# Kernel tuning notes

Measured on AMD Instinct MI355X. Metric: run time of the kernel, lower is better.

The kernel has to match this reference:

```python
import jax, jax.numpy as jnp
import numpy as np

H = 1024          # hidden_size
NH = 16           # num_attention_heads
HD = H // NH      # attention_head_size (= rotary_dim)
I = 4096          # intermediate_size
E = 8             # num_experts
TOPK = 2          # top_k_experts
EPS = 1e-12       # layer_norm_eps
B, S = 2, 2048


def setup_inputs() -> dict:
    key = jax.random.key(0)
    ks = jax.random.split(key, 12)
    sc = 0.02
    return {
        "hidden_states": jax.random.normal(ks[0], (B, S, H), dtype=jnp.float32),
        "Wq": jax.random.normal(ks[1], (H, H), dtype=jnp.float32) * sc,
        "Wk": jax.random.normal(ks[2], (H, H), dtype=jnp.float32) * sc,
        "Wv": jax.random.normal(ks[3], (H, H), dtype=jnp.float32) * sc,
        "Wd": jax.random.normal(ks[4], (H, H), dtype=jnp.float32) * sc,
        "bd": jnp.zeros((H,), dtype=jnp.float32),
        "ln1_g": jnp.ones((H,), dtype=jnp.float32),
        "ln1_b": jnp.zeros((H,), dtype=jnp.float32),
        "Wg": jax.random.normal(ks[5], (H, E), dtype=jnp.float32) * sc,
        "W1": jax.random.normal(ks[6], (E, H, I), dtype=jnp.float32) * sc,
        "W2": jax.random.normal(ks[7], (E, I, H), dtype=jnp.float32) * sc,
        "ln2_g": jnp.ones((H,), dtype=jnp.float32),
        "ln2_b": jnp.zeros((H,), dtype=jnp.float32),
    }


def _layernorm(x, g, b):
    mu = jnp.mean(x, axis=-1, keepdims=True)
    var = jnp.mean(jnp.square(x - mu), axis=-1, keepdims=True)
    return (x - mu) * jax.lax.rsqrt(var + EPS) * g + b


def _rotate_half(x):
    x1, x2 = x[..., : HD // 2], x[..., HD // 2 :]
    return jnp.concatenate((-x2, x1), axis=-1)


def _rope_cos_sin(seq_len, dtype):
    inv_freq = 1.0 / (10000.0 ** (jnp.arange(0, HD, 2, dtype=jnp.float32) / HD))
    t = jnp.arange(seq_len, dtype=jnp.float32)
    freqs = jnp.einsum("i,j->ij", t, inv_freq)          # [S, HD/2]
    emb = jnp.concatenate((freqs, freqs), axis=-1)        # [S, HD]
    return jnp.cos(emb).astype(dtype)[None, None], jnp.sin(emb).astype(dtype)[None, None]


def reference(hidden_states, Wq, Wk, Wv, Wd, bd, ln1_g, ln1_b, Wg, W1, W2, ln2_g, ln2_b):
    b, s, h = hidden_states.shape
    x = hidden_states

    # ---- multi-head attention with RoPE ----
    def heads(z):  # [B,S,H] -> [B,NH,S,HD]
        return z.reshape(b, s, NH, HD).transpose(0, 2, 1, 3)

    q = heads(x @ Wq)
    k = heads(x @ Wk)
    v = heads(x @ Wv)
    cos, sin = _rope_cos_sin(s, q.dtype)
    q = q * cos + _rotate_half(q) * sin
    k = k * cos + _rotate_half(k) * sin

    scores = jnp.einsum("bnqd,bnkd->bnqk", q, k) / jnp.sqrt(jnp.float32(HD)).astype(q.dtype)
    probs = jax.nn.softmax(scores, axis=-1)
    ctx = jnp.einsum("bnqk,bnkd->bnqd", probs, v)
    ctx = ctx.transpose(0, 2, 1, 3).reshape(b, s, h)

    attn_out = ctx @ Wd + bd
    hs = _layernorm(attn_out + x, ln1_g, ln1_b)  # residual + LN

    # ---- MoE ----
    T = b * s
    xt = hs.reshape(T, h)
    router_logits = xt @ Wg                                   # [T, E]
    probs_r = jax.nn.softmax(router_logits.astype(jnp.float32), axis=-1)
    rw, sel = jax.lax.top_k(probs_r, TOPK)                    # [T, K]
    rw = rw / jnp.sum(rw, axis=-1, keepdims=True)

    # aux load-balancing loss
    f_i = jnp.sum(jax.nn.one_hot(sel, E, dtype=jnp.float32), axis=(0, 1)) / T
    P_i = jnp.mean(probs_r, axis=0)
    aux_loss = E * jnp.sum(f_i * P_i)

    # per-token combine weights [T, E] (0 for unrouted experts)
    combine = jnp.zeros((T, E), dtype=jnp.float32)
    combine = combine.at[jnp.arange(T)[:, None], sel].add(rw)
    combine = combine.astype(xt.dtype)

    moe_out = jnp.zeros_like(xt)
    for e in range(E):  # small fixed expert loop
        ye = jax.nn.gelu(xt @ W1[e], approximate=False) @ W2[e]
        moe_out = moe_out + combine[:, e : e + 1] * ye
    moe_out = moe_out.reshape(b, s, h)

    out = _layernorm(hs + moe_out, ln2_g, ln2_b)
    return out, aux_loss
```

## Files before the change

kernel.cpp:

```cpp
#include <hip/hip_runtime.h>
#include <hip/hip_bf16.h>
#include <math.h>

#define H_ 1024
#define NH_ 16
#define HD_ 64
#define I_ 4096
#define E_ 8
#define B_ 2
#define S_ 2048
#define T_ 4096

#define MAXSLOTS 9216
#define MAXTILES 72

typedef __attribute__((ext_vector_type(8))) short short8v;
typedef __attribute__((ext_vector_type(4))) float f32x4;

#define GLOAD16(g, l) __builtin_amdgcn_global_load_lds((const __attribute__((address_space(1))) void*)(g), (__attribute__((address_space(3))) void*)(l), 16, 0, 0)

static __device__ inline unsigned short f2bf(float x) {
    __hip_bfloat16 h = __float2bfloat16(x);
    unsigned short u;
    __builtin_memcpy(&u, &h, 2);
    return u;
}
static __device__ inline float bf2f(unsigned short u) {
    __hip_bfloat16 h;
    __builtin_memcpy(&h, &u, 2);
    return __bfloat162float(h);
}

static __device__ inline float gelu_fast(float x) {
    float z  = x * 0.70710678118654752f;
    float az = fabsf(z);
    float t  = __builtin_amdgcn_rcpf(fmaf(0.3275911f, az, 1.f));
    float p  = fmaf(1.061405429f, t, -1.453152027f);
    p = fmaf(p, t, 1.421413741f);
    p = fmaf(p, t, -0.284496736f);
    p = fmaf(p, t, 0.254829592f);
    p = p * t;
    float e = __expf(-az*az);
    float er = 1.f - p*e;
    er = (z < 0.f) ? -er : er;
    return 0.5f * x * (1.f + er);
}

__global__ void zero_all(float* __restrict__ p, int n, float* __restrict__ misc16) {
    int i = blockIdx.x * blockDim.x + threadIdx.x;
    if (i < n) p[i] = 0.f;
    if (blockIdx.x == 0 && threadIdx.x < 16) misc16[threadIdx.x] = 0.f;
}

__global__ __launch_bounds__(256) void prep_inputs(
    const float* __restrict__ x,
    const float* __restrict__ Wq, const float* __restrict__ Wk,
    const float* __restrict__ Wv, const float* __restrict__ Wd,
    __hip_bfloat16* __restrict__ xa_hi, __hip_bfloat16* __restrict__ xa_lo,
    __hip_bfloat16* __restrict__ wqkv_h, __hip_bfloat16* __restrict__ wqkv_l,
    __hip_bfloat16* __restrict__ wd_h, __hip_bfloat16* __restrict__ wd_l)
{
    __shared__ float t[64][65];
    const int bid = blockIdx.x;
    const int tid = threadIdx.x;
    if (bid < 4096) {
        int i = bid * 256 + tid;
        float4 v = ((const float4*)x)[i];
        unsigned short h0 = f2bf(v.x), h1 = f2bf(v.y), h2 = f2bf(v.z), h3 = f2bf(v.w);
        unsigned short l0 = f2bf(v.x - bf2f(h0)), l1 = f2bf(v.y - bf2f(h1));
        unsigned short l2 = f2bf(v.z - bf2f(h2)), l3 = f2bf(v.w - bf2f(h3));
        uint2 ph = make_uint2((unsigned)h0 | ((unsigned)h1 << 16), (unsigned)h2 | ((unsigned)h3 << 16));
        uint2 pl = make_uint2((unsigned)l0 | ((unsigned)l1 << 16), (unsigned)l2 | ((unsigned)l3 << 16));
        *(uint2*)((char*)xa_hi + (size_t)i*8) = ph;
        *(uint2*)((char*)xa_lo + (size_t)i*8) = pl;
        return;
    }
    int tt = bid - 4096;
    int bx = tt & 15, by = (tt >> 4) & 15, z = tt >> 8;
    const float* in = (z==0) ? Wq : (z==1) ? Wk : (z==2) ? Wv : Wd;
    __hip_bfloat16* oh = (z<3) ? (wqkv_h + (size_t)z*1024*1024) : wd_h;
    __hip_bfloat16* ol = (z<3) ? (wqkv_l + (size_t)z*1024*1024) : wd_l;
    int k0 = by*64, n0 = bx*64;
    #pragma unroll
    for (int it=0; it<4; ++it) {
        int lin = it*256 + tid;
        int r = lin >> 4, c4 = (lin & 15) << 2;
        float4 v = *(const float4*)&in[(size_t)(k0+r)*1024 + n0 + c4];
        t[r][c4] = v.x; t[r][c4+1] = v.y; t[r][c4+2] = v.z; t[r][c4+3] = v.w;
    }
    __syncthreads();
    #pragma unroll
    for (int it=0; it<4; ++it) {
        int lin = it*256 + tid;
        int r = lin >> 4, c4 = (lin & 15) << 2;
        float v0 = t[c4][r], v1 = t[c4+1][r], v2 = t[c4+2][r], v3 = t[c4+3][r];
        ushort4 hh, ll;
        hh.x = f2bf(v0); hh.y = f2bf(v1); hh.z = f2bf(v2); hh.w = f2bf(v3);
        ll.x = f2bf(v0 - bf2f(hh.x)); ll.y = f2bf(v1 - bf2f(hh.y));
        ll.z = f2bf(v2 - bf2f(hh.z)); ll.w = f2bf(v3 - bf2f(hh.w));
        size_t o = (size_t)(n0+r)*1024 + k0 + c4;
        *(ushort4*)&oh[o] = hh;
        *(ushort4*)&ol[o] = ll;
    }
}

__global__ __launch_bounds__(256) void transpose_bf16(
    const float* __restrict__ in, __hip_bfloat16* __restrict__ outp, int K, int N)
{
    __shared__ float t[64][65];
    size_t eoff = (size_t)blockIdx.z * (size_t)K * (size_t)N;
    int k0 = blockIdx.y*64, n0 = blockIdx.x*64;
    int tid = threadIdx.x;
    #pragma unroll
    for (int it=0; it<4; ++it) {
        int lin = it*256 + tid;
        int r = lin >> 4, c4 = (lin & 15) << 2;
        float4 v = *(const float4*)&in[eoff + (size_t)(k0+r)*N + n0 + c4];
        t[r][c4] = v.x; t[r][c4+1] = v.y; t[r][c4+2] = v.z; t[r][c4+3] = v.w;
    }
    __syncthreads();
    #pragma unroll
    for (int it=0; it<4; ++it) {
        int lin = it*256 + tid;
        int r = lin >> 4, c4 = (lin & 15) << 2;
        ushort4 o;
        o.x = f2bf(t[c4][r]);   o.y = f2bf(t[c4+1][r]);
        o.z = f2bf(t[c4+2][r]); o.w = f2bf(t[c4+3][r]);
        *(ushort4*)&outp[eoff + (size_t)(n0+r)*K + k0 + c4] = o;
    }
}

template<bool BIAS>
__global__ __launch_bounds__(256, 2) void gemm_bf16x3(
    const __hip_bfloat16* __restrict__ Ah, const __hip_bfloat16* __restrict__ Al,
    const __hip_bfloat16* __restrict__ Bh, const __hip_bfloat16* __restrict__ Bl,
    float* __restrict__ C, const float* __restrict__ bias, int N, int K, int nbx)
{
    const int tid = threadIdx.x;
    const int w = tid >> 6, lane = tid & 63;
    const int wg = blockIdx.x;
    const int xcd = wg & 7, ix = wg >> 3;
    const int byc = (int)(gridDim.x >> 3) / nbx;
    const int by = xcd*byc + ix / nbx;
    const int bx = ix % nbx;

    __shared__ __align__(16) char smem[65536];
    const int AH = 0, AL = 16384, BH = 32768, BL = 49152;

    const int laneg = lane >> 3;
    const int k2sw = ((lane & 7) ^ laneg) << 4;
    const int l15 = lane & 15, l4 = lane >> 4;
    const int wr = w >> 1, wc = w & 1;

    f32x4 acc[4][4];
    #pragma unroll
    for (int m=0;m<4;m++)
        #pragma unroll
        for (int n=0;n<4;n++) acc[m][n] = (f32x4){0.f,0.f,0.f,0.f};

    for (int k0 = 0; k0 < K; k0 += 64) {
        __syncthreads();
        #pragma unroll
        for (int qq=0;qq<4;qq++) {
            int arow = by*128 + (w*4+qq)*8 + laneg;
            int brow = bx*128 + (w*4+qq)*8 + laneg;
            size_t aoff = ((size_t)arow*K + k0)*2 + k2sw;
            size_t boff = ((size_t)brow*K + k0)*2 + k2sw;
            GLOAD16((const char*)Ah + aoff, smem + AH + (w*4+qq)*1024);
            GLOAD16((const char*)Al + aoff, smem + AL + (w*4+qq)*1024);
            GLOAD16((const char*)Bh + boff, smem + BH + (w*4+qq)*1024);
            GLOAD16((const char*)Bl + boff, smem + BL + (w*4+qq)*1024);
        }
        __syncthreads();

        short8v ahf[4][2], alf[4][2], bhf[4][2], blf[4][2];
        #pragma unroll
        for (int m=0;m<4;m++) {
            int row = wr*64 + m*16 + l15;
            int rb = row << 7, rsw = (row & 7) << 4;
            #pragma unroll
            for (int s=0;s<2;s++) {
                int off = rb + ((s*64 + (l4<<4)) ^ rsw);
                ahf[m][s] = *(const short8v*)(smem + AH + off);
                alf[m][s] = *(const short8v*)(smem + AL + off);
            }
        }
        #pragma unroll
        for (int n=0;n<4;n++) {
            int row = wc*64 + n*16 + l15;
            int rb = row << 7, rsw = (row & 7) << 4;
            #pragma unroll
            for (int s=0;s<2;s++) {
                int off = rb + ((s*64 + (l4<<4)) ^ rsw);
                bhf[n][s] = *(const short8v*)(smem + BH + off);
                blf[n][s] = *(const short8v*)(smem + BL + off);
            }
        }
        #pragma unroll
        for (int m=0;m<4;m++)
            #pragma unroll
            for (int n=0;n<4;n++)
                #pragma unroll
                for (int s=0;s<2;s++) {
                    acc[m][n] = __builtin_amdgcn_mfma_f32_16x16x32_bf16(ahf[m][s], bhf[n][s], acc[m][n], 0, 0, 0);
                    acc[m][n] = __builtin_amdgcn_mfma_f32_16x16x32_bf16(ahf[m][s], blf[n][s], acc[m][n], 0, 0, 0);
                    acc[m][n] = __builtin_amdgcn_mfma_f32_16x16x32_bf16(alf[m][s], bhf[n][s], acc[m][n], 0, 0, 0);
                }
    }

    #pragma unroll
    for (int m=0;m<4;m++)
        #pragma unroll
        for (int j=0;j<4;j++) {
            int orow = by*128 + wr*64 + m*16 + l4*4 + j;
            #pragma unroll
            for (int n=0;n<4;n++) {
                int ocol = bx*128 + wc*64 + n*16 + l15;
                float v = acc[m][n][j];
                if (BIAS) v += bias[ocol];
                C[(size_t)orow*N + ocol] = v;
            }
        }
}

__global__ __launch_bounds__(256, 2) void fused_qkv_w12(
    const __hip_bfloat16* __restrict__ Ah, const __hip_bfloat16* __restrict__ Al,
    const __hip_bfloat16* __restrict__ Bh, const __hip_bfloat16* __restrict__ Bl,
    float* __restrict__ C,
    const float* __restrict__ W1, const float* __restrict__ W2,
    __hip_bfloat16* __restrict__ W1t, __hip_bfloat16* __restrict__ W2t)
{
    __shared__ __align__(16) char smem[65536];
    const int tid = threadIdx.x;
    const int bid = blockIdx.x;

    if (bid < 768) {
        const int N = 3072, K = 1024;
        const int w = tid >> 6, lane = tid & 63;
        const int xcd = bid & 7, ix = bid >> 3;
        const int by = xcd*4 + ix / 24;
        const int bx = ix % 24;
        const int AH = 0, AL = 16384, BH = 32768, BL = 49152;
        const int laneg = lane >> 3;
        const int k2sw = ((lane & 7) ^ laneg) << 4;
        const int l15 = lane & 15, l4 = lane >> 4;
        const int wr = w >> 1, wc = w & 1;

        f32x4 acc[4][4];
        #pragma unroll
        for (int m=0;m<4;m++)
            #pragma unroll
            for (int n=0;n<4;n++) acc[m][n] = (f32x4){0.f,0.f,0.f,0.f};

        for (int k0 = 0; k0 < K; k0 += 64) {
            __syncthreads();
            #pragma unroll
            for (int qq=0;qq<4;qq++) {
                int arow = by*128 + (w*4+qq)*8 + laneg;
                int brow = bx*128 + (w*4+qq)*8 + laneg;
                size_t aoff = ((size_t)arow*K + k0)*2 + k2sw;
                size_t boff = ((size_t)brow*K + k0)*2 + k2sw;
                GLOAD16((const char*)Ah + aoff, smem + AH + (w*4+qq)*1024);
                GLOAD16((const char*)Al + aoff, smem + AL + (w*4+qq)*1024);
                GLOAD16((const char*)Bh + boff, smem + BH + (w*4+qq)*1024);
                GLOAD16((const char*)Bl + boff, smem + BL + (w*4+qq)*1024);
            }
            __syncthreads();

            short8v ahf[4][2], alf[4][2], bhf[4][2], blf[4][2];
            #pragma unroll
            for (int m=0;m<4;m++) {
                int row = wr*64 + m*16 + l15;
                int rb = row << 7, rsw = (row & 7) << 4;
                #pragma unroll
                for (int s=0;s<2;s++) {
                    int off = rb + ((s*64 + (l4<<4)) ^ rsw);
                    ahf[m][s] = *(const short8v*)(smem + AH + off);
                    alf[m][s] = *(const short8v*)(smem + AL + off);
                }
            }
            #pragma unroll
            for (int n=0;n<4;n++) {
                int row = wc*64 + n*16 + l15;
                int rb = row << 7, rsw = (row & 7) << 4;
                #pragma unroll
                for (int s=0;s<2;s++) {
                    int off = rb + ((s*64 + (l4<<4)) ^ rsw);
                    bhf[n][s] = *(const short8v*)(smem + BH + off);
                    blf[n][s] = *(const short8v*)(smem + BL + off);
                }
            }
            #pragma unroll
            for (int m=0;m<4;m++)
                #pragma unroll
                for (int n=0;n<4;n++)
                    #pragma unroll
                    for (int s=0;s<2;s++) {
                        acc[m][n] = __builtin_amdgcn_mfma_f32_16x16x32_bf16(ahf[m][s], bhf[n][s], acc[m][n], 0, 0, 0);
                        acc[m][n] = __builtin_amdgcn_mfma_f32_16x16x32_bf16(ahf[m][s], blf[n][s], acc[m][n], 0, 0, 0);
                        acc[m][n] = __builtin_amdgcn_mfma_f32_16x16x32_bf16(alf[m][s], bhf[n][s], acc[m][n], 0, 0, 0);
                    }
        }

        #pragma unroll
        for (int m=0;m<4;m++)
            #pragma unroll
            for (int j=0;j<4;j++) {
                int orow = by*128 + wr*64 + m*16 + l4*4 + j;
                #pragma unroll
                for (int n=0;n<4;n++) {
                    int ocol = bx*128 + wc*64 + n*16 + l15;
                    C[(size_t)orow*N + ocol] = acc[m][n][j];
                }
            }
        return;
    }

    int t = bid - 768;
    const float* src;
    __hip_bfloat16* dst;
    int K, N;
    if (t < 8192) { src = W1; dst = W1t; K = 1024; N = 4096; }
    else          { t -= 8192; src = W2; dst = W2t; K = 4096; N = 1024; }
    const int nb_n = N >> 6;
    int bx = t % nb_n;
    int rest = t / nb_n;
    int by = rest % (K >> 6);
    int bz = rest / (K >> 6);
    size_t eoff = (size_t)bz * (size_t)K * (size_t)N;
    int k0 = by*64, n0 = bx*64;
    float (*tt)[65] = (float(*)[65])smem;
    #pragma unroll
    for (int it=0; it<4; ++it) {
        int lin = it*256 + tid;
        int r = lin >> 4, c4 = (lin & 15) << 2;
        float4 v = *(const float4*)&src[eoff + (size_t)(k0+r)*N + n0 + c4];
        tt[r][c4] = v.x; tt[r][c4+1] = v.y; tt[r][c4+2] = v.z; tt[r][c4+3] = v.w;
    }
    __syncthreads();
    #pragma unroll
    for (int it=0; it<4; ++it) {
        int lin = it*256 + tid;
        int r = lin >> 4, c4 = (lin & 15) << 2;
        ushort4 o;
        o.x = f2bf(tt[c4][r]);   o.y = f2bf(tt[c4+1][r]);
        o.z = f2bf(tt[c4+2][r]); o.w = f2bf(tt[c4+3][r]);
        *(ushort4*)&dst[eoff + (size_t)(n0+r)*K + k0 + c4] = o;
    }
}

template<int MODE, bool PE>
__global__ __launch_bounds__(256) void moe_mfma(
    const __hip_bfloat16* __restrict__ A,
    const __hip_bfloat16* __restrict__ Bt,
    __hip_bfloat16* __restrict__ y1,
    float* __restrict__ moe_out,
    const int* __restrict__ slot_token,
    const float* __restrict__ slot_w,
    const int* __restrict__ tile_expert,
    const int* __restrict__ cnt_ptr,
    const int* __restrict__ base_ptr,
    int N, int K, int nbx)
{
    const int tid = threadIdx.x;
    const int w = tid >> 6, lane = tid & 63;

    int bx, slot0, y1row0;
    const __hip_bfloat16* Bp;
    if (PE) {
        bx = blockIdx.x;
        int tloc = blockIdx.y;
        if ((tloc << 7) >= *cnt_ptr) return;
        slot0 = *base_ptr + (tloc << 7);
        y1row0 = tloc << 7;
        Bp = Bt;
    } else {
        const int wg = blockIdx.x;
        const int xcd = wg & 7, ix = wg >> 3;
        const int byc = (int)(gridDim.x >> 3) / nbx;
        int gt = xcd*byc + ix % byc;
        bx = ix / byc;
        if (gt >= *cnt_ptr) return;
        int e = tile_expert[gt];
        Bp = Bt + (size_t)e * (size_t)K * (size_t)N;
        slot0 = gt << 7;
        y1row0 = gt << 7;
    }

    __shared__ __align__(16) char smem[32768];

    const int laneg = lane >> 3;
    const int k2sw = ((lane & 7) ^ laneg) << 4;

    int tokq[4];
    if (MODE == 2) {
        #pragma unroll
        for (int qq=0;qq<4;qq++) {
            int t0 = slot_token[slot0 + (w*4+qq)*8 + laneg];
            tokq[qq] = t0 < 0 ? 0 : t0;
        }
    }

    f32x4 acc[4][4];
    #pragma unroll
    for (int m=0;m<4;m++)
        #pragma unroll
        for (int n=0;n<4;n++) acc[m][n] = (f32x4){0.f,0.f,0.f,0.f};

    const int l15 = lane & 15;
    const int l4  = lane >> 4;
    const int wr = w >> 1, wc = w & 1;

    for (int k0 = 0; k0 < K; k0 += 64) {
        __syncthreads();
        #pragma unroll
        for (int qq=0;qq<4;qq++) {
            const char* ga;
            if (MODE == 2) {
                ga = (const char*)A + (((size_t)tokq[qq])*K + k0)*2 + k2sw;
            } else {
                int row = y1row0 + (w*4+qq)*8 + laneg;
                ga = (const char*)A + ((size_t)row*K + k0)*2 + k2sw;
            }
            GLOAD16(ga, smem + (w*4+qq)*1024);
        }
        #pragma unroll
        for (int qq=0;qq<4;qq++) {
            int row = bx*128 + (w*4+qq)*8 + laneg;
            const char* gb = (const char*)Bp + ((size_t)row*K + k0)*2 + k2sw;
            GLOAD16(gb, smem + 16384 + (w*4+qq)*1024);
        }
        __syncthreads();

        short8v a_frag[4][2], b_frag[4][2];
        #pragma unroll
        for (int m=0;m<4;m++) {
            int row = wr*64 + m*16 + l15;
            int rb = row << 7;
            #pragma unroll
            for (int s=0;s<2;s++) {
                int off = rb + ((s*64 + (l4<<4)) ^ ((row&7)<<4));
                a_frag[m][s] = *(const short8v*)(smem + off);
            }
        }
        #pragma unroll
        for (int n=0;n<4;n++) {
            int row = wc*64 + n*16 + l15;
            int rb = row << 7;
            #pragma unroll
            for (int s=0;s<2;s++) {
                int off = rb + ((s*64 + (l4<<4)) ^ ((row&7)<<4));
                b_frag[n][s] = *(const short8v*)(smem + 16384 + off);
            }
        }
        #pragma unroll
        for (int m=0;m<4;m++)
            #pragma unroll
            for (int n=0;n<4;n++) {
                acc[m][n] = __builtin_amdgcn_mfma_f32_16x16x32_bf16(a_frag[m][0], b_frag[n][0], acc[m][n], 0, 0, 0);
                acc[m][n] = __builtin_amdgcn_mfma_f32_16x16x32_bf16(a_frag[m][1], b_frag[n][1], acc[m][n], 0, 0, 0);
            }
    }

    if (MODE == 3) {
        #pragma unroll
        for (int m=0;m<4;m++) {
            #pragma unroll
            for (int j=0;j<4;j++) {
                int orow = wr*64 + m*16 + l4*4 + j;
                int slot = slot0 + orow;
                int tok = slot_token[slot];
                if (tok < 0) continue;
                float sw = slot_w[slot];
                #pragma unroll
                for (int n=0;n<4;n++) {
                    int ocol = bx*128 + wc*64 + n*16 + l15;
                    atomicAdd(&moe_out[(size_t)tok*H_ + ocol], sw * acc[m][n][j]);
                }
            }
        }
    } else {
        __syncthreads();
        #pragma unroll
        for (int m=0;m<4;m++)
            #pragma unroll
            for (int j=0;j<4;j++) {
                int orow = wr*64 + m*16 + l4*4 + j;
                #pragma unroll
                for (int n=0;n<4;n++) {
                    int ocol = wc*64 + n*16 + l15;
                    unsigned short g = f2bf(gelu_fast(acc[m][n][j]));
                    *(unsigned short*)(smem + orow*256 + ocol*2) = g;
                }
            }
        __syncthreads();
        #pragma unroll
        for (int s=0;s<8;s++) {
            int row = w*32 + s*4 + l4;
            short8v v = *(const short8v*)(smem + row*256 + l15*16);
            *(short8v*)((char*)y1 + ((size_t)(y1row0 + row)*N + bx*128 + l15*8)*2) = v;
        }
    }
}

__global__ __launch_bounds__(256) void rope_vsplit(
    const float* __restrict__ qkv,
    __hip_bfloat16* __restrict__ qh, __hip_bfloat16* __restrict__ ql,
    __hip_bfloat16* __restrict__ kh, __hip_bfloat16* __restrict__ kl,
    __hip_bfloat16* __restrict__ vth, __hip_bfloat16* __restrict__ vtl)
{
    __shared__ float t[64][65];
    const int bid = blockIdx.x;
    const int tid = threadIdx.x;
    if (bid < 8192) {
        int idx = bid * 256 + tid;
        int i = idx & 31;
        int n = (idx >> 5) & (NH_-1);
        int tk = idx >> 9;
        int b = tk >> 11;
        int pos = tk & (S_ - 1);
        float inv = exp2f((float)i * (-13.287712379549449f / 32.f));
        float ang = (float)pos * inv;
        float c = cosf(ang), s = sinf(ang);
        size_t base = (size_t)tk*3072 + (size_t)n*64;
        size_t obase = ((size_t)(b*NH_ + n)*S_ + pos)*64;

        float q1 = qkv[base+i], q2 = qkv[base+i+32];
        float qo1 = (q1*c - q2*s)*0.125f;
        float qo2 = (q2*c + q1*s)*0.125f;
        unsigned short h1 = f2bf(qo1), h2 = f2bf(qo2);
        qh[obase+i]    = *(__hip_bfloat16*)&h1;
        qh[obase+i+32] = *(__hip_bfloat16*)&h2;
        unsigned short lo1 = f2bf(qo1 - bf2f(h1)), lo2 = f2bf(qo2 - bf2f(h2));
        ql[obase+i]    = *(__hip_bfloat16*)&lo1;
        ql[obase+i+32] = *(__hip_bfloat16*)&lo2;

        float k1 = qkv[base+1024+i], k2 = qkv[base+1024+i+32];
        float ko1 = k1*c - k2*s;
        float ko2 = k2*c + k1*s;
        unsigned short kh1 = f2bf(ko1), kh2 = f2bf(ko2);
        kh[obase+i]    = *(__hip_bfloat16*)&kh1;
        kh[obase+i+32] = *(__hip_bfloat16*)&kh2;
        unsigned short kl1 = f2bf(ko1 - bf2f(kh1)), kl2 = f2bf(ko2 - bf2f(kh2));
        kl[obase+i]    = *(__hip_bfloat16*)&kl1;
        kl[obase+i+32] = *(__hip_bfloat16*)&kl2;
        return;
    }
    int tt = bid - 8192;
    const int s0 = (tt & 31)*64;
    const int hn = (tt >> 5) & 15;
    const int b  = tt >> 9;
    #pragma unroll
    for (int it=0; it<4; ++it) {
        int lin = it*256 + tid;
        int r = lin >> 4, c4 = (lin & 15) << 2;
        float4 vv = *(const float4*)&qkv[(size_t)(b*S_ + s0 + r)*3072 + 2048 + hn*64 + c4];
        t[r][c4] = vv.x; t[r][c4+1] = vv.y; t[r][c4+2] = vv.z; t[r][c4+3] = vv.w;
    }
    __syncthreads();
    size_t obase = (size_t)(b*NH_ + hn)*64*S_;
    #pragma unroll
    for (int it=0; it<4; ++it) {
        int lin = it*256 + tid;
        int d = lin >> 4, c4 = (lin & 15) << 2;
        float v0 = t[c4][d], v1 = t[c4+1][d], v2 = t[c4+2][d], v3 = t[c4+3][d];
        ushort4 hh, ll;
        hh.x = f2bf(v0); hh.y = f2bf(v1); hh.z = f2bf(v2); hh.w = f2bf(v3);
        ll.x = f2bf(v0 - bf2f(hh.x)); ll.y = f2bf(v1 - bf2f(hh.y));
        ll.z = f2bf(v2 - bf2f(hh.z)); ll.w = f2bf(v3 - bf2f(hh.w));
        size_t o = obase + (size_t)d*S_ + s0 + c4;
        *(ushort4*)&vth[o] = hh;
        *(ushort4*)&vtl[o] = ll;
    }
}

__global__ __launch_bounds__(256) void attn_mfma(
    const __hip_bfloat16* __restrict__ qh, const __hip_bfloat16* __restrict__ ql,
    const __hip_bfloat16* __restrict__ kh, const __hip_bfloat16* __restrict__ kl,
    const __hip_bfloat16* __restrict__ vth, const __hip_bfloat16* __restrict__ vtl,
    __hip_bfloat16* __restrict__ ctx_hi, __hip_bfloat16* __restrict__ ctx_lo)
{
    const int wg = blockIdx.x;
    const int xcd = wg & 7;
    const int ix = wg >> 3;
    const int head = xcd*4 + (ix >> 5);
    const int qt = ix & 31;
    const int b = head >> 4, hn = head & 15;

    const int tid = threadIdx.x;
    const int w = tid >> 6, lane = tid & 63;
    const int l15 = lane & 15, l4 = lane >> 4;
    const int laneg = lane >> 3;
    const int k2sw = ((lane & 7) ^ laneg) << 4;

    __shared__ __align__(16) char smem[32768];
    const int KHo = 0, KLo = 8192, VHo = 16384, VLo = 24576;
    const int PHo = 0, PLo = 8192;

    const size_t kbase = (size_t)head*S_*64;
    const size_t vbase = (size_t)head*64*S_;

    #pragma unroll
    for (int qq=0;qq<2;qq++) {
        int c = w*2 + qq;
        int row = qt*64 + c*8 + laneg;
        size_t off = (kbase + (size_t)row*64)*2 + k2sw;
        GLOAD16((const char*)qh + off, smem + KHo + c*1024);
        GLOAD16((const char*)ql + off, smem + KLo + c*1024);
    }
    __syncthreads();
    short8v qhf[2], qlf[2];
    {
        int row = w*16 + l15;
        int rsw = (row & 7) << 4;
        #pragma unroll
        for (int s=0;s<2;s++) {
            int off = row*128 + ((s*64 + l4*16) ^ rsw);
            qhf[s] = *(const short8v*)(smem + KHo + off);
            qlf[s] = *(const short8v*)(smem + KLo + off);
        }
    }

    f32x4 acc[4];
    #pragma unroll
    for (int db=0;db<4;db++) acc[db] = (f32x4){0.f,0.f,0.f,0.f};
    float lrun[4] = {0.f, 0.f, 0.f, 0.f};

    for (int kt=0; kt<S_/64; ++kt) {
        __syncthreads();
        #pragma unroll
        for (int qq=0;qq<2;qq++) {
            int c = w*2 + qq;
            int r8 = c*8 + laneg;
            size_t koff = (kbase + (size_t)(kt*64 + r8)*64)*2 + k2sw;
            GLOAD16((const char*)kh + koff, smem + KHo + c*1024);
            GLOAD16((const char*)kl + koff, smem + KLo + c*1024);
            size_t voff = (vbase + (size_t)r8*S_ + kt*64)*2 + k2sw;
            GLOAD16((const char*)vth + voff, smem + VHo + c*1024);
            GLOAD16((const char*)vtl + voff, smem + VLo + c*1024);
        }
        __syncthreads();

        f32x4 s_acc[4];
        #pragma unroll
        for (int cb=0;cb<4;cb++) {
            s_acc[cb] = (f32x4){0.f,0.f,0.f,0.f};
            int row = cb*16 + l15;
            int rsw = (row & 7) << 4;
            #pragma unroll
            for (int s=0;s<2;s++) {
                int off = row*128 + ((s*64 + l4*16) ^ rsw);
                short8v khf = *(const short8v*)(smem + KHo + off);
                short8v klf = *(const short8v*)(smem + KLo + off);
                s_acc[cb] = __builtin_amdgcn_mfma_f32_16x16x32_bf16(qhf[s], khf, s_acc[cb], 0, 0, 0);
                s_acc[cb] = __builtin_amdgcn_mfma_f32_16x16x32_bf16(qhf[s], klf, s_acc[cb], 0, 0, 0);
                s_acc[cb] = __builtin_amdgcn_mfma_f32_16x16x32_bf16(qlf[s], khf, s_acc[cb], 0, 0, 0);
            }
        }
        __syncthreads();

        #pragma unroll
        for (int cb=0;cb<4;cb++)
            #pragma unroll
            for (int j=0;j<4;j++) {
                float p = __expf(s_acc[cb][j]);
                lrun[j] += p;
                int prow = w*16 + l4*4 + j;
                unsigned short hh = f2bf(p);
                unsigned short ll = f2bf(p - bf2f(hh));
                int off = prow*128 + (((cb*16 + l15)*2) ^ ((prow&7)<<4));
                *(unsigned short*)(smem + PHo + off) = hh;
                *(unsigned short*)(smem + PLo + off) = ll;
            }
        asm volatile("s_waitcnt lgkmcnt(0)" ::: "memory");
        __builtin_amdgcn_sched_barrier(0);

        short8v pah[2], pal[2];
        {
            int row = w*16 + l15;
            int rsw = (row & 7) << 4;
            #pragma unroll
            for (int s=0;s<2;s++) {
                int off = row*128 + ((s*64 + l4*16) ^ rsw);
                pah[s] = *(const short8v*)(smem + PHo + off);
                pal[s] = *(const short8v*)(smem + PLo + off);
            }
        }
        #pragma unroll
        for (int db=0;db<4;db++) {
            int row = db*16 + l15;
            int rsw = (row & 7) << 4;
            #pragma unroll
            for (int s=0;s<2;s++) {
                int off = row*128 + ((s*64 + l4*16) ^ rsw);
                short8v vhf = *(const short8v*)(smem + VHo + off);
                short8v vlf = *(const short8v*)(smem + VLo + off);
                acc[db] = __builtin_amdgcn_mfma_f32_16x16x32_bf16(pah[s], vhf, acc[db], 0, 0, 0);
                acc[db] = __builtin_amdgcn_mfma_f32_16x16x32_bf16(pah[s], vlf, acc[db], 0, 0, 0);
                acc[db] = __builtin_amdgcn_mfma_f32_16x16x32_bf16(pal[s], vhf, acc[db], 0, 0, 0);
            }
        }
    }

    #pragma unroll
    for (int j=0;j<4;j++) {
        float s = lrun[j];
        #pragma unroll
        for (int m=8;m;m>>=1) s += __shfl_xor(s, m);
        lrun[j] = s;
    }

    #pragma unroll
    for (int db=0;db<4;db++)
        #pragma unroll
        for (int j=0;j<4;j++) {
            int qrow = qt*64 + w*16 + l4*4 + j;
            float o = acc[db][j] / lrun[j];
            unsigned short hh = f2bf(o);
            unsigned short ll = f2bf(o - bf2f(hh));
            size_t oidx = (size_t)(b*S_ + qrow)*H_ + hn*64 + db*16 + l15;
            ctx_hi[oidx] = *(__hip_bfloat16*)&hh;
            ctx_lo[oidx] = *(__hip_bfloat16*)&ll;
        }
}

__global__ __launch_bounds__(256) void ln_kernel(
    const float* __restrict__ a, const float* __restrict__ res,
    const float* __restrict__ g, const float* __restrict__ beta,
    float* __restrict__ out, __hip_bfloat16* __restrict__ outb)
{
    int row = blockIdx.x, tid = threadIdx.x;
    const float4 va = ((const float4*)(a + (size_t)row*H_))[tid];
    const float4 vr = ((const float4*)(res + (size_t)row*H_))[tid];
    float x0=va.x+vr.x, x1=va.y+vr.y, x2=va.z+vr.z, x3=va.w+vr.w;
    float s  = x0+x1+x2+x3;
    float ss = x0*x0 + x1*x1 + x2*x2 + x3*x3;
    #pragma unroll
    for (int off=32; off; off>>=1) { s += __shfl_xor(s, off); ss += __shfl_xor(ss, off); }
    __shared__ float red[8];
    if ((tid&63)==0) { red[tid>>6]=s; red[4+(tid>>6)]=ss; }
    __syncthreads();
    if (tid==0) { red[0]=red[0]+red[1]+red[2]+red[3]; red[4]=red[4]+red[5]+red[6]+red[7]; }
    __syncthreads();
    float mu  = red[0] * (1.f/H_);
    float var = red[4] * (1.f/H_) - mu*mu;
    float rs = rsqrtf(fmaxf(var, 0.f) + 1e-12f);
    const float4 vg = ((const float4*)g)[tid];
    const float4 vb = ((const float4*)beta)[tid];
    float4 vo;
    vo.x = (x0-mu)*rs*vg.x + vb.x;
    vo.y = (x1-mu)*rs*vg.y + vb.y;
    vo.z = (x2-mu)*rs*vg.z + vb.z;
    vo.w = (x3-mu)*rs*vg.w + vb.w;
    ((float4*)(out + (size_t)row*H_))[tid] = vo;
    if (outb) {
        unsigned int p0 = (unsigned)f2bf(vo.x) | ((unsigned)f2bf(vo.y) << 16);
        unsigned int p1 = (unsigned)f2bf(vo.z) | ((unsigned)f2bf(vo.w) << 16);
        ((uint2*)(outb + (size_t)row*H_))[tid] = make_uint2(p0, p1);
    }
}

__global__ __launch_bounds__(256) void router_kernel(
    const float* __restrict__ hs, const float* __restrict__ Wg,
    int* __restrict__ tok_e, float* __restrict__ tok_w,
    int* __restrict__ counts, float* __restrict__ P_sum)
{
    const int w = threadIdx.x >> 6, lane = threadIdx.x & 63;
    float psum[E_];
    int cnt[E_];
    #pragma unroll
    for (int e=0;e<E_;e++){ psum[e]=0.f; cnt[e]=0; }

    for (int it=0; it<16; ++it) {
        int t = blockIdx.x*64 + it*4 + w;
        const float* row = hs + (size_t)t * H_;
        float acc[E_];
        #pragma unroll
        for (int e=0;e<E_;e++) acc[e]=0.f;
        for (int i16=0; i16<16; ++i16) {
            int i = i16*64 + lane;
            float xv = row[i];
            const float* wg = Wg + (size_t)i*E_;
            #pragma unroll
            for (int e=0;e<E_;e++) acc[e] = fmaf(xv, wg[e], acc[e]);
        }
        #pragma unroll
        for (int e=0;e<E_;e++) {
            float vv = acc[e];
            #pragma unroll
            for (int off=32; off; off>>=1) vv += __shfl_xor(vv, off);
            acc[e] = vv;
        }
        float mx = acc[0];
        #pragma unroll
        for (int e=1;e<E_;e++) mx = fmaxf(mx, acc[e]);
        float p[E_], se=0.f;
        #pragma unroll
        for (int e=0;e<E_;e++){ p[e] = __expf(acc[e]-mx); se += p[e]; }
        float isv = 1.f/se;
        #pragma unroll
        for (int e=0;e<E_;e++){ p[e]*=isv; psum[e] += p[e]; }
        int e1=0;
        #pragma unroll
        for (int e=1;e<E_;e++) if (p[e] > p[e1]) e1=e;
        int e2 = (e1==0)?1:0;
        #pragma unroll
        for (int e=0;e<E_;e++) if (e!=e1 && p[e] > p[e2]) e2=e;
        #pragma unroll
        for (int e=0;e<E_;e++) cnt[e] += (e==e1?1:0) + (e==e2?1:0);
        if (lane==0) {
            float w1=p[e1], w2=p[e2], si=1.f/(w1+w2);
            tok_e[t*2]=e1; tok_e[t*2+1]=e2;
            tok_w[t*2]=w1*si; tok_w[t*2+1]=w2*si;
        }
    }
    if (lane==0) {
        #pragma unroll
        for (int e=0;e<E_;e++) {
            atomicAdd(&P_sum[e], psum[e]);
            atomicAdd(&counts[e], cnt[e]);
        }
    }
}

__global__ void router_finalize(
    const int* __restrict__ counts, const float* __restrict__ P_sum,
    int* __restrict__ base, int* __restrict__ cursor,
    int* __restrict__ cnt_pad, int* __restrict__ ntiles,
    int* __restrict__ slot_token, int* __restrict__ tile_expert,
    float* __restrict__ aux_out)
{
    __shared__ int sbase[E_+1];
    if (threadIdx.x == 0) {
        int bacc = 0;
        float aux = 0.f;
        for (int e=0;e<E_;e++) {
            sbase[e] = bacc; base[e] = bacc;
            int cp = (counts[e] + 127) & ~127;
            cnt_pad[e] = cp;
            bacc += cp;
            cursor[e] = 0;
            aux += ((float)counts[e]/(float)T_) * (P_sum[e]/(float)T_);
        }
        sbase[E_] = bacc;
        *ntiles = bacc >> 7;
        *aux_out = (float)E_ * aux;
    }
    __syncthreads();
    for (int sIdx = (int)threadIdx.x; sIdx < MAXSLOTS; sIdx += (int)blockDim.x)
        slot_token[sIdx] = -1;
    for (int tt = (int)threadIdx.x; tt < MAXTILES; tt += (int)blockDim.x) {
        int s = tt*128;
        int e = E_-1;
        for (int qe=0; qe<E_; ++qe) if (s < sbase[qe+1]) { e = qe; break; }
        tile_expert[tt] = e;
    }
}

__global__ void scatter_slots(
    const int* __restrict__ tok_e, const float* __restrict__ tok_w,
    const int* __restrict__ base, int* __restrict__ cursor,
    int* __restrict__ slot_token, float* __restrict__ slot_w)
{
    int t = blockIdx.x*blockDim.x + threadIdx.x;
    if (t >= T_) return;
    #pragma unroll
    for (int j=0;j<2;j++) {
        int e = tok_e[t*2+j];
        int pos = atomicAdd(&cursor[e], 1);
        int s = base[e] + pos;
        slot_token[s] = t;
        slot_w[s] = tok_w[t*2+j];
    }
}

extern "C" void kernel_launch(void* const* d_in, const int* in_sizes, int n_in,
                              void* d_out, int out_size, void* d_ws, size_t ws_size,
                              hipStream_t stream)
{
    const float* x    = (const float*)d_in[0];
    const float* Wq   = (const float*)d_in[1];
    const float* Wk   = (const float*)d_in[2];
    const float* Wv   = (const float*)d_in[3];
    const float* Wd   = (const float*)d_in[4];
    const float* bd   = (const float*)d_in[5];
    const float* ln1g = (const float*)d_in[6];
    const float* ln1b = (const float*)d_in[7];
    const float* Wg   = (const float*)d_in[8];
    const float* W1   = (const float*)d_in[9];
    const float* W2   = (const float*)d_in[10];
    const float* ln2g = (const float*)d_in[11];
    const float* ln2b = (const float*)d_in[12];
    float* out = (float*)d_out;

    float* f0 = (float*)d_ws;
    const size_t M1 = 1u << 20;
    float* qkv      = f0;
    float* attn_out = f0 + 12*M1;
    float* hs       = f0;
    float* moe_out  = f0 + 4*M1;
    __hip_bfloat16* hs_b = (__hip_bfloat16*)(f0 + 16*M1);

    float* misc = f0 + 18*M1;
    int*   misc_i = (int*)misc;
    int*   tok_e   = misc_i;
    float* tok_w   = misc + 8192;
    int*   slot_tok= misc_i + 16384;
    float* slot_w  = misc + 25600;
    int*   counts  = misc_i + 34816;
    float* P_sum   = misc + 34824;
    int*   cursor  = misc_i + 34832;
    int*   basep   = misc_i + 34840;
    int*   cnt_pad = misc_i + 34848;
    int*   ntiles  = misc_i + 34856;
    int*   tile_ex = misc_i + 34857;

    float* off_p = f0 + 18*M1 + 65536;
    __hip_bfloat16* xa_hi = (__hip_bfloat16*)(off_p);
    __hip_bfloat16* xa_lo = (__hip_bfloat16*)(off_p + 2*M1);
    __hip_bfloat16* at_qh = (__hip_bfloat16*)(off_p + 4*M1);
    __hip_bfloat16* at_ql = (__hip_bfloat16*)(off_p + 6*M1);
    __hip_bfloat16* at_kh = (__hip_bfloat16*)(off_p + 8*M1);
    __hip_bfloat16* at_kl = (__hip_bfloat16*)(off_p + 10*M1);
    __hip_bfloat16* at_vh = (__hip_bfloat16*)(off_p + 12*M1);
    __hip_bfloat16* at_vl = (__hip_bfloat16*)(off_p + 14*M1);
    __hip_bfloat16* wqkv_h = (__hip_bfloat16*)(off_p + 16*M1);
    __hip_bfloat16* wqkv_l = (__hip_bfloat16*)(off_p + 16*M1 + 3*(M1/2));
    __hip_bfloat16* wd_h = (__hip_bfloat16*)(off_p + 19*M1);
    __hip_bfloat16* wd_l = (__hip_bfloat16*)(off_p + 19*M1 + M1/2);

    const bool FULL = ws_size >= (size_t)300*1024*1024;
    __hip_bfloat16* W1t = (__hip_bfloat16*)(off_p + 20*M1);
    __hip_bfloat16* W2t = (__hip_bfloat16*)(off_p + 36*M1);
    __hip_bfloat16* y1F = (__hip_bfloat16*)(off_p);
    float* wreg = off_p + 4*M1;

    dim3 blk(256);

    prep_inputs<<<dim3(5120), blk, 0, stream>>>(x, Wq, Wk, Wv, Wd, xa_hi, xa_lo, wqkv_h, wqkv_l, wd_h, wd_l);

    if (FULL) {
        fused_qkv_w12<<<dim3(768 + 8192 + 8192), blk, 0, stream>>>(
            xa_hi, xa_lo, wqkv_h, wqkv_l, qkv, W1, W2, W1t, W2t);
    } else {
        gemm_bf16x3<false><<<dim3(768), blk, 0, stream>>>(xa_hi, xa_lo, wqkv_h, wqkv_l, qkv, nullptr, 3072, H_, 24);
    }

    rope_vsplit<<<dim3(8192 + 1024), blk, 0, stream>>>(qkv, at_qh, at_ql, at_kh, at_kl, at_vh, at_vl);

    attn_mfma<<<dim3(B_*NH_*(S_/64)), blk, 0, stream>>>(at_qh, at_ql, at_kh, at_kl, at_vh, at_vl, xa_hi, xa_lo);

    gemm_bf16x3<true><<<dim3(256), blk, 0, stream>>>(xa_hi, xa_lo, wd_h, wd_l, attn_out, bd, H_, H_, 8);

    zero_all<<<dim3((T_*H_)/256), blk, 0, stream>>>(moe_out, T_*H_, misc + 34816);

    ln_kernel<<<T_, blk, 0, stream>>>(attn_out, x, ln1g, ln1b, hs, hs_b);

    router_kernel<<<T_/64, blk, 0, stream>>>(hs, Wg, tok_e, tok_w, counts, P_sum);
    router_finalize<<<1, blk, 0, stream>>>(counts, P_sum, basep, cursor, cnt_pad, ntiles,
                                           slot_tok, tile_ex, out + (size_t)T_*H_);
    scatter_slots<<<T_/256, blk, 0, stream>>>(tok_e, tok_w, basep, cursor, slot_tok, slot_w);

    if (FULL) {
        moe_mfma<2,false><<<dim3(MAXTILES*32), blk, 0, stream>>>(
            hs_b, W1t, y1F, nullptr, slot_tok, slot_w, tile_ex, ntiles, nullptr, I_, H_, 32);
        moe_mfma<3,false><<<dim3(MAXTILES*8), blk, 0, stream>>>(
            y1F, W2t, nullptr, moe_out, slot_tok, slot_w, tile_ex, ntiles, nullptr, H_, I_, 8);
    } else {
        __hip_bfloat16* w1t = (__hip_bfloat16*)wreg;
        __hip_bfloat16* w2t = (__hip_bfloat16*)(wreg + 2*M1);
        __hip_bfloat16* y1  = (__hip_bfloat16*)(wreg + 4*M1);
        for (int e=0; e<E_; ++e) {
            transpose_bf16<<<dim3(I_/64, H_/64, 1), blk, 0, stream>>>(W1 + (size_t)e*H_*I_, w1t, H_, I_);
            moe_mfma<2,true><<<dim3(I_/128, 32), blk, 0, stream>>>(
                hs_b, w1t, y1, nullptr, slot_tok, slot_w, nullptr, cnt_pad+e, basep+e, I_, H_, 0);
            transpose_bf16<<<dim3(H_/64, I_/64, 1), blk, 0, stream>>>(W2 + (size_t)e*I_*H_, w2t, I_, H_);
            moe_mfma<3,true><<<dim3(H_/128, 32), blk, 0, stream>>>(
                y1, w2t, nullptr, moe_out, slot_tok, slot_w, nullptr, cnt_pad+e, basep+e, H_, I_, 0);
        }
    }

    ln_kernel<<<T_, blk, 0, stream>>>(moe_out, hs, ln2g, ln2b, out, nullptr);
}
```

Measured before the change: 756.5 us.

## Process two query tiles per attention block and fuse zeroing into Wd GEMM

The attention kernel now handles 128 query rows per workgroup as two 64-row sub-tiles. Each K/V tile loaded into shared memory is reused for both, which halves K/V global traffic and the grid size. Separately, zeroing of the MoE output buffer moves into extra blocks of a dedicated Wd GEMM kernel, removing one kernel launch. The trade-offs are higher register pressure from the doubled accumulators and Q fragments, fewer workgroups to fill the GPU during attention, and extra barriers in the Q preload.

```diff
diff --git a/kernel.cpp b/kernel.cpp
--- a/kernel.cpp
+++ b/kernel.cpp
@@ -44,12 +44,6 @@
     float er = 1.f - p*e;
     er = (z < 0.f) ? -er : er;
     return 0.5f * x * (1.f + er);
-}
-
-__global__ void zero_all(float* __restrict__ p, int n, float* __restrict__ misc16) {
-    int i = blockIdx.x * blockDim.x + threadIdx.x;
-    if (i < n) p[i] = 0.f;
-    if (blockIdx.x == 0 && threadIdx.x < 16) misc16[threadIdx.x] = 0.f;
 }
 
 __global__ __launch_bounds__(256) void prep_inputs(
@@ -219,6 +213,103 @@
                 float v = acc[m][n][j];
                 if (BIAS) v += bias[ocol];
                 C[(size_t)orow*N + ocol] = v;
+            }
+        }
+}
+
+__global__ __launch_bounds__(256, 2) void wd_gemm_zero(
+    const __hip_bfloat16* __restrict__ Ah, const __hip_bfloat16* __restrict__ Al,
+    const __hip_bfloat16* __restrict__ Bh, const __hip_bfloat16* __restrict__ Bl,
+    float* __restrict__ C, const float* __restrict__ bias,
+    float* __restrict__ moe_out, float* __restrict__ misc16)
+{
+    const int bid = blockIdx.x;
+    const int tid = threadIdx.x;
+    if (bid >= 256) {
+        int z = bid - 256;
+        ((float4*)moe_out)[z*256 + tid] = (float4){0.f,0.f,0.f,0.f};
+        if (z == 0 && tid < 16) misc16[tid] = 0.f;
+        return;
+    }
+    const int N = 1024, K = 1024;
+    const int w = tid >> 6, lane = tid & 63;
+    const int xcd = bid & 7, ix = bid >> 3;
+    const int by = xcd*4 + ix / 8;
+    const int bx = ix % 8;
+
+    __shared__ __align__(16) char smem[65536];
+    const int AH = 0, AL = 16384, BH = 32768, BL = 49152;
+
+    const int laneg = lane >> 3;
+    const int k2sw = ((lane & 7) ^ laneg) << 4;
+    const int l15 = lane & 15, l4 = lane >> 4;
+    const int wr = w >> 1, wc = w & 1;
+
+    f32x4 acc[4][4];
+    #pragma unroll
+    for (int m=0;m<4;m++)
+        #pragma unroll
+        for (int n=0;n<4;n++) acc[m][n] = (f32x4){0.f,0.f,0.f,0.f};
+
+    for (int k0 = 0; k0 < K; k0 += 64) {
+        __syncthreads();
+        #pragma unroll
+        for (int qq=0;qq<4;qq++) {
+            int arow = by*128 + (w*4+qq)*8 + laneg;
+            int brow = bx*128 + (w*4+qq)*8 + laneg;
+            size_t aoff = ((size_t)arow*K + k0)*2 + k2sw;
+            size_t boff = ((size_t)brow*K + k0)*2 + k2sw;
+            GLOAD16((const char*)Ah + aoff, smem + AH + (w*4+qq)*1024);
+            GLOAD16((const char*)Al + aoff, smem + AL + (w*4+qq)*1024);
+            GLOAD16((const char*)Bh + boff, smem + BH + (w*4+qq)*1024);
+            GLOAD16((const char*)Bl + boff, smem + BL + (w*4+qq)*1024);
+        }
+        __syncthreads();
+
+        short8v ahf[4][2], alf[4][2], bhf[4][2], blf[4][2];
+        #pragma unroll
+        for (int m=0;m<4;m++) {
+            int row = wr*64 + m*16 + l15;
+            int rb = row << 7, rsw = (row & 7) << 4;
+            #pragma unroll
+            for (int s=0;s<2;s++) {
+                int off = rb + ((s*64 + (l4<<4)) ^ rsw);
+                ahf[m][s] = *(const short8v*)(smem + AH + off);
+                alf[m][s] = *(const short8v*)(smem + AL + off);
+            }
+        }
+        #pragma unroll
+        for (int n=0;n<4;n++) {
+            int row = wc*64 + n*16 + l15;
+            int rb = row << 7, rsw = (row & 7) << 4;
+            #pragma unroll
+            for (int s=0;s<2;s++) {
+                int off = rb + ((s*64 + (l4<<4)) ^ rsw);
+                bhf[n][s] = *(const short8v*)(smem + BH + off);
+                blf[n][s] = *(const short8v*)(smem + BL + off);
+            }
+        }
+        #pragma unroll
+        for (int m=0;m<4;m++)
+            #pragma unroll
+            for (int n=0;n<4;n++)
+                #pragma unroll
+                for (int s=0;s<2;s++) {
+                    acc[m][n] = __builtin_amdgcn_mfma_f32_16x16x32_bf16(ahf[m][s], bhf[n][s], acc[m][n], 0, 0, 0);
+                    acc[m][n] = __builtin_amdgcn_mfma_f32_16x16x32_bf16(ahf[m][s], blf[n][s], acc[m][n], 0, 0, 0);
+                    acc[m][n] = __builtin_amdgcn_mfma_f32_16x16x32_bf16(alf[m][s], bhf[n][s], acc[m][n], 0, 0, 0);
+                }
+    }
+
+    #pragma unroll
+    for (int m=0;m<4;m++)
+        #pragma unroll
+        for (int j=0;j<4;j++) {
+            int orow = by*128 + wr*64 + m*16 + l4*4 + j;
+            #pragma unroll
+            for (int n=0;n<4;n++) {
+                int ocol = bx*128 + wc*64 + n*16 + l15;
+                C[(size_t)orow*N + ocol] = acc[m][n][j] + bias[ocol];
             }
         }
 }
@@ -583,8 +674,8 @@
     const int wg = blockIdx.x;
     const int xcd = wg & 7;
     const int ix = wg >> 3;
-    const int head = xcd*4 + (ix >> 5);
-    const int qt = ix & 31;
+    const int head = xcd*4 + (ix >> 4);
+    const int qt = ix & 15;
     const int b = head >> 4, hn = head & 15;
 
     const int tid = threadIdx.x;
@@ -600,34 +691,39 @@
     const size_t kbase = (size_t)head*S_*64;
     const size_t vbase = (size_t)head*64*S_;
 
-    #pragma unroll
-    for (int qq=0;qq<2;qq++) {
-        int c = w*2 + qq;
-        int row = qt*64 + c*8 + laneg;
-        size_t off = (kbase + (size_t)row*64)*2 + k2sw;
-        GLOAD16((const char*)qh + off, smem + KHo + c*1024);
-        GLOAD16((const char*)ql + off, smem + KLo + c*1024);
-    }
-    __syncthreads();
-    short8v qhf[2], qlf[2];
-    {
-        int row = w*16 + l15;
-        int rsw = (row & 7) << 4;
-        #pragma unroll
-        for (int s=0;s<2;s++) {
-            int off = row*128 + ((s*64 + l4*16) ^ rsw);
-            qhf[s] = *(const short8v*)(smem + KHo + off);
-            qlf[s] = *(const short8v*)(smem + KLo + off);
-        }
-    }
-
-    f32x4 acc[4];
-    #pragma unroll
-    for (int db=0;db<4;db++) acc[db] = (f32x4){0.f,0.f,0.f,0.f};
-    float lrun[4] = {0.f, 0.f, 0.f, 0.f};
+    short8v qhf[2][2], qlf[2][2];
+    #pragma unroll
+    for (int m=0;m<2;m++) {
+        #pragma unroll
+        for (int qq=0;qq<2;qq++) {
+            int c = w*2 + qq;
+            int row = qt*128 + m*64 + c*8 + laneg;
+            size_t off = (kbase + (size_t)row*64)*2 + k2sw;
+            GLOAD16((const char*)qh + off, smem + KHo + c*1024);
+            GLOAD16((const char*)ql + off, smem + KLo + c*1024);
+        }
+        __syncthreads();
+        {
+            int row = w*16 + l15;
+            int rsw = (row & 7) << 4;
+            #pragma unroll
+            for (int s=0;s<2;s++) {
+                int off = row*128 + ((s*64 + l4*16) ^ rsw);
+                qhf[m][s] = *(const short8v*)(smem + KHo + off);
+                qlf[m][s] = *(const short8v*)(smem + KLo + off);
+            }
+        }
+        __syncthreads();
+    }
+
+    f32x4 acc[2][4];
+    #pragma unroll
+    for (int m=0;m<2;m++)
+        #pragma unroll
+        for (int db=0;db<4;db++) acc[m][db] = (f32x4){0.f,0.f,0.f,0.f};
+    float lrun[2][4] = {{0.f,0.f,0.f,0.f},{0.f,0.f,0.f,0.f}};
 
     for (int kt=0; kt<S_/64; ++kt) {
-        __syncthreads();
         #pragma unroll
         for (int qq=0;qq<2;qq++) {
             int c = w*2 + qq;
@@ -641,10 +737,11 @@
         }
         __syncthreads();
 
-        f32x4 s_acc[4];
+        f32x4 s_acc[2][4];
         #pragma unroll
         for (int cb=0;cb<4;cb++) {
-            s_acc[cb] = (f32x4){0.f,0.f,0.f,0.f};
+            s_acc[0][cb] = (f32x4){0.f,0.f,0.f,0.f};
+            s_acc[1][cb] = (f32x4){0.f,0.f,0.f,0.f};
             int row = cb*16 + l15;
             int rsw = (row & 7) << 4;
             #pragma unroll
@@ -652,76 +749,86 @@
                 int off = row*128 + ((s*64 + l4*16) ^ rsw);
                 short8v khf = *(const short8v*)(smem + KHo + off);
                 short8v klf = *(const short8v*)(smem + KLo + off);
-                s_acc[cb] = __builtin_amdgcn_mfma_f32_16x16x32_bf16(qhf[s], khf, s_acc[cb], 0, 0, 0);
-                s_acc[cb] = __builtin_amdgcn_mfma_f32_16x16x32_bf16(qhf[s], klf, s_acc[cb], 0, 0, 0);
-                s_acc[cb] = __builtin_amdgcn_mfma_f32_16x16x32_bf16(qlf[s], khf, s_acc[cb], 0, 0, 0);
-            }
-        }
-        __syncthreads();
-
-        #pragma unroll
-        for (int cb=0;cb<4;cb++)
+                s_acc[0][cb] = __builtin_amdgcn_mfma_f32_16x16x32_bf16(qhf[0][s], khf, s_acc[0][cb], 0, 0, 0);
+                s_acc[0][cb] = __builtin_amdgcn_mfma_f32_16x16x32_bf16(qhf[0][s], klf, s_acc[0][cb], 0, 0, 0);
+                s_acc[0][cb] = __builtin_amdgcn_mfma_f32_16x16x32_bf16(qlf[0][s], khf, s_acc[0][cb], 0, 0, 0);
+                s_acc[1][cb] = __builtin_amdgcn_mfma_f32_16x16x32_bf16(qhf[1][s], khf, s_acc[1][cb], 0, 0, 0);
+                s_acc[1][cb] = __builtin_amdgcn_mfma_f32_16x16x32_bf16(qhf[1][s], klf, s_acc[1][cb], 0, 0, 0);
+                s_acc[1][cb] = __builtin_amdgcn_mfma_f32_16x16x32_bf16(qlf[1][s], khf, s_acc[1][cb], 0, 0, 0);
+            }
+        }
+        __syncthreads();
+
+        #pragma unroll
+        for (int m=0;m<2;m++) {
+            #pragma unroll
+            for (int cb=0;cb<4;cb++)
+                #pragma unroll
+                for (int j=0;j<4;j++) {
+                    float p = __expf(s_acc[m][cb][j]);
+                    lrun[m][j] += p;
+                    int prow = w*16 + l4*4 + j;
+                    unsigned short hh = f2bf(p);
+                    unsigned short ll = f2bf(p - bf2f(hh));
+                    int off = prow*128 + (((cb*16 + l15)*2) ^ ((prow&7)<<4));
+                    *(unsigned short*)(smem + PHo + off) = hh;
+                    *(unsigned short*)(smem + PLo + off) = ll;
+                }
+            asm volatile("s_waitcnt lgkmcnt(0)" ::: "memory");
+            __builtin_amdgcn_sched_barrier(0);
+
+            short8v pah[2], pal[2];
+            {
+                int row = w*16 + l15;
+                int rsw = (row & 7) << 4;
+                #pragma unroll
+                for (int s=0;s<2;s++) {
+                    int off = row*128 + ((s*64 + l4*16) ^ rsw);
+                    pah[s] = *(const short8v*)(smem + PHo + off);
+                    pal[s] = *(const short8v*)(smem + PLo + off);
+                }
+            }
+            #pragma unroll
+            for (int db=0;db<4;db++) {
+                int row = db*16 + l15;
+                int rsw = (row & 7) << 4;
+                #pragma unroll
+                for (int s=0;s<2;s++) {
+                    int off = row*128 + ((s*64 + l4*16) ^ rsw);
+                    short8v vhf = *(const short8v*)(smem + VHo + off);
+                    short8v vlf = *(const short8v*)(smem + VLo + off);
+                    acc[m][db] = __builtin_amdgcn_mfma_f32_16x16x32_bf16(pah[s], vhf, acc[m][db], 0, 0, 0);
+                    acc[m][db] = __builtin_amdgcn_mfma_f32_16x16x32_bf16(pah[s], vlf, acc[m][db], 0, 0, 0);
+                    acc[m][db] = __builtin_amdgcn_mfma_f32_16x16x32_bf16(pal[s], vhf, acc[m][db], 0, 0, 0);
+                }
+            }
+            __builtin_amdgcn_sched_barrier(0);
+        }
+        __syncthreads();
+    }
+
+    #pragma unroll
+    for (int m=0;m<2;m++) {
+        #pragma unroll
+        for (int j=0;j<4;j++) {
+            float s = lrun[m][j];
+            #pragma unroll
+            for (int mk=8;mk;mk>>=1) s += __shfl_xor(s, mk);
+            lrun[m][j] = s;
+        }
+        #pragma unroll
+        for (int db=0;db<4;db++)
             #pragma unroll
             for (int j=0;j<4;j++) {
-                float p = __expf(s_acc[cb][j]);
-                lrun[j] += p;
-                int prow = w*16 + l4*4 + j;
-                unsigned short hh = f2bf(p);
-                unsigned short ll = f2bf(p - bf2f(hh));
-                int off = prow*128 + (((cb*16 + l15)*2) ^ ((prow&7)<<4));
-                *(unsigned short*)(smem + PHo + off) = hh;
-                *(unsigned short*)(smem + PLo + off) = ll;
-            }
-        asm volatile("s_waitcnt lgkmcnt(0)" ::: "memory");
-        __builtin_amdgcn_sched_barrier(0);
-
-        short8v pah[2], pal[2];
-        {
-            int row = w*16 + l15;
-            int rsw = (row & 7) << 4;
-            #pragma unroll
-            for (int s=0;s<2;s++) {
-                int off = row*128 + ((s*64 + l4*16) ^ rsw);
-                pah[s] = *(const short8v*)(smem + PHo + off);
-                pal[s] = *(const short8v*)(smem + PLo + off);
-            }
-        }
-        #pragma unroll
-        for (int db=0;db<4;db++) {
-            int row = db*16 + l15;
-            int rsw = (row & 7) << 4;
-            #pragma unroll
-            for (int s=0;s<2;s++) {
-                int off = row*128 + ((s*64 + l4*16) ^ rsw);
-                short8v vhf = *(const short8v*)(smem + VHo + off);
-                short8v vlf = *(const short8v*)(smem + VLo + off);
-                acc[db] = __builtin_amdgcn_mfma_f32_16x16x32_bf16(pah[s], vhf, acc[db], 0, 0, 0);
-                acc[db] = __builtin_amdgcn_mfma_f32_16x16x32_bf16(pah[s], vlf, acc[db], 0, 0, 0);
-                acc[db] = __builtin_amdgcn_mfma_f32_16x16x32_bf16(pal[s], vhf, acc[db], 0, 0, 0);
-            }
-        }
-    }
-
-    #pragma unroll
-    for (int j=0;j<4;j++) {
-        float s = lrun[j];
-        #pragma unroll
-        for (int m=8;m;m>>=1) s += __shfl_xor(s, m);
-        lrun[j] = s;
-    }
-
-    #pragma unroll
-    for (int db=0;db<4;db++)
-        #pragma unroll
-        for (int j=0;j<4;j++) {
-            int qrow = qt*64 + w*16 + l4*4 + j;
-            float o = acc[db][j] / lrun[j];
-            unsigned short hh = f2bf(o);
-            unsigned short ll = f2bf(o - bf2f(hh));
-            size_t oidx = (size_t)(b*S_ + qrow)*H_ + hn*64 + db*16 + l15;
-            ctx_hi[oidx] = *(__hip_bfloat16*)&hh;
-            ctx_lo[oidx] = *(__hip_bfloat16*)&ll;
-        }
+                int qrow = qt*128 + m*64 + w*16 + l4*4 + j;
+                float o = acc[m][db][j] / lrun[m][j];
+                unsigned short hh = f2bf(o);
+                unsigned short ll = f2bf(o - bf2f(hh));
+                size_t oidx = (size_t)(b*S_ + qrow)*H_ + hn*64 + db*16 + l15;
+                ctx_hi[oidx] = *(__hip_bfloat16*)&hh;
+                ctx_lo[oidx] = *(__hip_bfloat16*)&ll;
+            }
+    }
 }
 
 __global__ __launch_bounds__(256) void ln_kernel(
@@ -948,11 +1055,9 @@
 
     rope_vsplit<<<dim3(8192 + 1024), blk, 0, stream>>>(qkv, at_qh, at_ql, at_kh, at_kl, at_vh, at_vl);
 
-    attn_mfma<<<dim3(B_*NH_*(S_/64)), blk, 0, stream>>>(at_qh, at_ql, at_kh, at_kl, at_vh, at_vl, xa_hi, xa_lo);
-
-    gemm_bf16x3<true><<<dim3(256), blk, 0, stream>>>(xa_hi, xa_lo, wd_h, wd_l, attn_out, bd, H_, H_, 8);
-
-    zero_all<<<dim3((T_*H_)/256), blk, 0, stream>>>(moe_out, T_*H_, misc + 34816);
+    attn_mfma<<<dim3(B_*NH_*(S_/128)), blk, 0, stream>>>(at_qh, at_ql, at_kh, at_kl, at_vh, at_vl, xa_hi, xa_lo);
+
+    wd_gemm_zero<<<dim3(256 + 4096), blk, 0, stream>>>(xa_hi, xa_lo, wd_h, wd_l, attn_out, bd, moe_out, misc + 34816);
 
     ln_kernel<<<T_, blk, 0, stream>>>(attn_out, x, ln1g, ln1b, hs, hs_b);
 
```

New measurement: 750.9 us. Within noise of the previous version (-0.7%).
